# Performance work log

Hardware: AMD Instinct MI355X
Metric: run time of the kernel (lower is better)

## Reference

```python
import jax, jax.numpy as jnp
import numpy as np

EP = 1e-4
EPMAX = 30.0
RTOL, ATOL = 1e-5, 1e-8  # torch.allclose defaults


def _safe(n):
    return jnp.where(n == 0, 1.0, n)


def _rigid_from_3(x):
    # x: (L, 3, 3) -> rot (L,3,3) rows e1,e2,e3 ; origin (L,3)
    x1, x2, x3 = x[:, 0], x[:, 1], x[:, 2]
    v1 = x3 - x2
    v2 = x1 - x2
    e1 = v1 / (jnp.linalg.norm(v1, axis=-1, keepdims=True) + 1e-3)
    u2 = v2 - e1 * jnp.einsum('ld,ld->l', e1, v2)[:, None]
    e2 = u2 / (jnp.linalg.norm(u2, axis=-1, keepdims=True) + 1e-8)
    e3 = jnp.cross(e1, e2)
    return jnp.stack([e1, e2, e3], axis=1), x2


def _merge_frames(rot, trans, ii, jj):
    # Vectorized merge_coordinate_systems over all selected pairs (ii, jj).
    O_A, O_B = trans[ii], trans[jj]          # (P,3)
    RA, RB = rot[ii], rot[jj]                # (P,3,3)
    close = jnp.all(jnp.abs(O_A - O_B) <= ATOL + RTOL * jnp.abs(O_B), axis=-1)
    d = O_B - O_A
    nd = jnp.linalg.norm(d, axis=-1)
    X_new = d / _safe(nd)[:, None]
    Z_add = RA[:, 2] + RB[:, 2]
    Z_sub = RA[:, 2] - RB[:, 2]
    na = jnp.linalg.norm(Z_add, axis=-1)
    ns = jnp.linalg.norm(Z_sub, axis=-1)
    Z_new = jnp.where((na > ns)[:, None], Z_add / _safe(na)[:, None], Z_sub / _safe(ns)[:, None])
    Y_new = jnp.cross(Z_new, X_new)
    nan_bad = jnp.any(jnp.isnan(Y_new), axis=-1)
    flip = jnp.einsum('pd,pd->p', jnp.cross(X_new, Y_new), Z_new) < 0
    Y_new = jnp.where(flip[:, None], -Y_new, Y_new)
    R_new = jnp.stack([X_new, Y_new, Z_new], axis=1)  # (P,3,3)
    O_new = 0.5 * (O_A + O_B)
    bad = close | (nd == 0) | (na == 0) | (ns == 0) | nan_bad
    R_out = jnp.where(bad[:, None, None], RA, R_new)
    O_out = jnp.where(bad[:, None], O_A, O_new)
    return jnp.concatenate([rot, R_out], axis=0), jnp.concatenate([trans, O_out], axis=0)


def _frame_transform(points, rot, tran):
    # points: (N,3); rot: (F,3,3); tran: (F,3) -> (N,F,3)
    diff = points[:, None, :] - tran[None, :, :]
    return jnp.einsum('nfd,fed->nfe', diff, rot)


def setup_inputs():
    key = jax.random.key(0)
    k0, k1, k2, k3 = jax.random.split(key, 4)
    L = 1024
    coor = 5.0 * jax.random.normal(k0, (L, 3, 3), jnp.float32)
    # valid orthonormal frames from random points
    rot, _ = _rigid_from_3(5.0 * jax.random.normal(k1, (L, 3, 3), jnp.float32))
    trans = 5.0 * jax.random.normal(k2, (L, 3), jnp.float32)
    target = 5.0 * jax.random.normal(k3, (L, 3, 3), jnp.float32)
    idx = np.arange(L)
    band = idx[None, :] - idx[:, None]
    matrix = ((band > 0) & (band <= 8)).astype(np.int32)  # ~8k contact pairs
    return {"coor": coor, "rot": rot, "trans": trans, "target": target,
            "matrix": jnp.asarray(matrix)}


def reference(coor, rot, trans, target, matrix):
    m = np.asarray(matrix)
    ii_np, jj_np = np.nonzero(np.triu(m, 1) == 1)
    ii, jj = jnp.asarray(ii_np), jnp.asarray(jj_np)
    p_rot, p_tran = _merge_frames(rot, trans, ii, jj)
    pred_x2 = _frame_transform(coor.reshape(-1, 3), p_rot, p_tran)   # (N,F,3)
    t_rot0, t_tran0 = _rigid_from_3(target)
    t_rot, t_tran = _merge_frames(t_rot0, t_tran0, ii, jj)
    tx = _frame_transform(target.reshape(-1, 3), t_rot, t_tran)     # (N,F,3)
    errmap = jnp.sqrt(jnp.sum((pred_x2 - tx) ** 2 + EP, axis=-1))
    return jnp.mean(jnp.minimum(errmap, EPMAX))
```

## Files before the change

kernel.cpp:

```cpp
#include <hip/hip_runtime.h>

#define EPV    0.0001f
#define EPMAXV 30.0f
#define RTOLV  1e-5f
#define ATOLV  1e-8f
#define NPART  1024
#define CHUNK  112

#define PIN(x) asm volatile("" : "+v"(x))


__device__ inline void write_rec(float* __restrict__ rec,
                                 const float Rp[9], const float Op[3],
                                 const float Rt[9], const float Ot[3]) {
    float P[9], N[9];
#pragma unroll
    for (int k = 0; k < 9; k++) { P[k] = Rp[k]; N[k] = -Rt[k]; }
    float kx = -(P[0] * Op[0] + P[1] * Op[1] + P[2] * Op[2]
               + N[0] * Ot[0] + N[1] * Ot[1] + N[2] * Ot[2]);
    float ky = -(P[3] * Op[0] + P[4] * Op[1] + P[5] * Op[2]
               + N[3] * Ot[0] + N[4] * Ot[1] + N[5] * Ot[2]);
    float kz = -(P[6] * Op[0] + P[7] * Op[1] + P[8] * Op[2]
               + N[6] * Ot[0] + N[7] * Ot[1] + N[8] * Ot[2]);
    float4* r4 = (float4*)rec;
    r4[0] = make_float4(P[0], P[1], P[2], P[3]);
    r4[1] = make_float4(P[4], P[5], P[6], P[7]);
    r4[2] = make_float4(P[8], N[0], N[1], N[2]);
    r4[3] = make_float4(N[3], N[4], N[5], N[6]);
    r4[4] = make_float4(N[7], N[8], kx, ky);
    r4[5] = make_float4(kz, 0.f, 0.f, 0.f);
}

__global__ void k_prep(const int* __restrict__ m, int L, unsigned int* __restrict__ rowcnt,
                       const float* __restrict__ rot, const float* __restrict__ trans,
                       const float* __restrict__ target, int nrb,
                       float* __restrict__ pF, float* __restrict__ tF,
                       float* __restrict__ rec) {
    if ((int)blockIdx.x < nrb) {
        int i = blockIdx.x * 4 + (threadIdx.x >> 6);
        if (i >= L) return;
        int lane = threadIdx.x & 63;
        const int4* row4 = (const int4*)(m + (size_t)i * L);
        unsigned int c = 0;
        for (int b = lane; b * 4 < L; b += 64) {
            int4 v = row4[b];
            int j = b * 4;
            c += (unsigned)((j + 0 > i) & (v.x == 1)) + (unsigned)((j + 1 > i) & (v.y == 1))
               + (unsigned)((j + 2 > i) & (v.z == 1)) + (unsigned)((j + 3 > i) & (v.w == 1));
        }
#pragma unroll
        for (int off = 1; off < 64; off <<= 1) c += __shfl_xor(c, off, 64);
        if (lane == 0) rowcnt[i] = c;
        return;
    }
    int l = ((int)blockIdx.x - nrb) * 256 + threadIdx.x;
    if (l >= L) return;
    float Rp[9], Op[3];
#pragma unroll
    for (int k = 0; k < 9; k++) Rp[k] = rot[l * 9 + k];
#pragma unroll
    for (int k = 0; k < 3; k++) Op[k] = trans[l * 3 + k];
    float* pf = pF + l * 12;
#pragma unroll
    for (int k = 0; k < 9; k++) pf[k] = Rp[k];
#pragma unroll
    for (int k = 0; k < 3; k++) pf[9 + k] = Op[k];
    const float* tg = target + l * 9;
    float x1x = tg[0], x1y = tg[1], x1z = tg[2];
    float x2x = tg[3], x2y = tg[4], x2z = tg[5];
    float x3x = tg[6], x3y = tg[7], x3z = tg[8];
    float v1x = x3x - x2x, v1y = x3y - x2y, v1z = x3z - x2z;
    float v2x = x1x - x2x, v2y = x1y - x2y, v2z = x1z - x2z;
    float n1 = sqrtf(v1x * v1x + v1y * v1y + v1z * v1z) + 0.001f;
    float e1x = v1x / n1, e1y = v1y / n1, e1z = v1z / n1;
    float c = e1x * v2x + e1y * v2y + e1z * v2z;
    float u2x = v2x - c * e1x, u2y = v2y - c * e1y, u2z = v2z - c * e1z;
    float n2 = sqrtf(u2x * u2x + u2y * u2y + u2z * u2z) + 1e-8f;
    float e2x = u2x / n2, e2y = u2y / n2, e2z = u2z / n2;
    float Rt[9], Ot[3];
    Rt[0] = e1x; Rt[1] = e1y; Rt[2] = e1z;
    Rt[3] = e2x; Rt[4] = e2y; Rt[5] = e2z;
    Rt[6] = e1y * e2z - e1z * e2y;
    Rt[7] = e1z * e2x - e1x * e2z;
    Rt[8] = e1x * e2y - e1y * e2x;
    Ot[0] = x2x; Ot[1] = x2y; Ot[2] = x2z;
    float* tf = tF + l * 12;
#pragma unroll
    for (int k = 0; k < 9; k++) tf[k] = Rt[k];
#pragma unroll
    for (int k = 0; k < 3; k++) tf[9 + k] = Ot[k];
    write_rec(rec + (size_t)l * 24, Rp, Op, Rt, Ot);
}

__device__ inline void merge_frames(const float* __restrict__ A, const float* __restrict__ B,
                                    float R[9], float O[3]) {
    const float* RA = A; const float* OA = A + 9;
    const float* RB = B; const float* OB = B + 9;
    bool close = (fabsf(OA[0] - OB[0]) <= ATOLV + RTOLV * fabsf(OB[0])) &&
                 (fabsf(OA[1] - OB[1]) <= ATOLV + RTOLV * fabsf(OB[1])) &&
                 (fabsf(OA[2] - OB[2]) <= ATOLV + RTOLV * fabsf(OB[2]));
    float d0 = OB[0] - OA[0], d1 = OB[1] - OA[1], d2 = OB[2] - OA[2];
    float nd = sqrtf(d0 * d0 + d1 * d1 + d2 * d2);
    float nds = (nd == 0.f) ? 1.f : nd;
    float X0 = d0 / nds, X1 = d1 / nds, X2 = d2 / nds;
    float Za0 = RA[6] + RB[6], Za1 = RA[7] + RB[7], Za2 = RA[8] + RB[8];
    float Zs0 = RA[6] - RB[6], Zs1 = RA[7] - RB[7], Zs2 = RA[8] - RB[8];
    float na = sqrtf(Za0 * Za0 + Za1 * Za1 + Za2 * Za2);
    float ns = sqrtf(Zs0 * Zs0 + Zs1 * Zs1 + Zs2 * Zs2);
    float nas = (na == 0.f) ? 1.f : na;
    float nss = (ns == 0.f) ? 1.f : ns;
    float Z0, Z1, Z2;
    if (na > ns) { Z0 = Za0 / nas; Z1 = Za1 / nas; Z2 = Za2 / nas; }
    else         { Z0 = Zs0 / nss; Z1 = Zs1 / nss; Z2 = Zs2 / nss; }
    float Y0 = Z1 * X2 - Z2 * X1;
    float Y1 = Z2 * X0 - Z0 * X2;
    float Y2 = Z0 * X1 - Z1 * X0;
    bool nanbad = (Y0 != Y0) || (Y1 != Y1) || (Y2 != Y2);
    float C0 = X1 * Y2 - X2 * Y1;
    float C1 = X2 * Y0 - X0 * Y2;
    float C2 = X0 * Y1 - X1 * Y0;
    float dotv = C0 * Z0 + C1 * Z1 + C2 * Z2;
    if (dotv < 0.f) { Y0 = -Y0; Y1 = -Y1; Y2 = -Y2; }
    bool bad = close || (nd == 0.f) || (na == 0.f) || (ns == 0.f) || nanbad;
    if (bad) {
#pragma unroll
        for (int k = 0; k < 9; k++) R[k] = RA[k];
#pragma unroll
        for (int k = 0; k < 3; k++) O[k] = OA[k];
    } else {
        R[0] = X0; R[1] = X1; R[2] = X2;
        R[3] = Y0; R[4] = Y1; R[5] = Y2;
        R[6] = Z0; R[7] = Z1; R[8] = Z2;
        O[0] = 0.5f * (OA[0] + OB[0]);
        O[1] = 0.5f * (OA[1] + OB[1]);
        O[2] = 0.5f * (OA[2] + OB[2]);
    }
}

__global__ void k_fillmerge(const int* __restrict__ m, int L,
                            const unsigned int* __restrict__ rowcnt,
                            unsigned int* __restrict__ count, int cap,
                            const float* __restrict__ pF, const float* __restrict__ tF,
                            float* __restrict__ rec) {
    int i = blockIdx.x * 4 + (threadIdx.x >> 6);
    int lane = threadIdx.x & 63;

    if (blockIdx.x == 0 && (threadIdx.x >> 6) == 0) {
        unsigned int t = 0;
        for (int r = lane; r < L; r += 64) t += rowcnt[r];
#pragma unroll
        for (int off = 1; off < 64; off <<= 1) t += __shfl_xor(t, off, 64);
        if (lane == 0) *count = t;
    }
    if (i >= L) return;

    unsigned int p = 0;
    for (int r = lane; r < i; r += 64) p += rowcnt[r];
#pragma unroll
    for (int off = 1; off < 64; off <<= 1) p += __shfl_xor(p, off, 64);
    unsigned int base = p;

    const int* row = m + (size_t)i * L;
    unsigned long long lt = (lane == 0) ? 0ull : ((1ull << lane) - 1ull);
    for (int j0 = 0; j0 < L; j0 += 64) {
        int j = j0 + lane;
        bool v = (j < L) && (j > i) && (row[j] == 1);
        unsigned long long b = __ballot(v);
        if (v) {
            unsigned int pos = base + (unsigned int)__popcll(b & lt);
            if (pos < (unsigned int)cap) {
                float Rp[9], Op[3], Rt[9], Ot[3];
                merge_frames(pF + i * 12, pF + j * 12, Rp, Op);
                merge_frames(tF + i * 12, tF + j * 12, Rt, Ot);
                write_rec(rec + (size_t)(L + pos) * 24, Rp, Op, Rt, Ot);
            }
        }
        base += (unsigned int)__popcll(b);
    }
}

__global__ __launch_bounds__(256, 4)
void k_main(const float* __restrict__ coor, const float* __restrict__ target,
            const float* __restrict__ rec, const unsigned int* __restrict__ count,
            int cap, int L, int Npts, double* __restrict__ partials) {
    __shared__ float4 sC[CHUNK];
    __shared__ float4 sT[CHUNK];
    __shared__ float sRed[4];
    unsigned int cnt = *count;
    if (cnt > (unsigned int)cap) cnt = (unsigned int)cap;
    int F = L + (int)cnt;
    int nfb = (F + 255) >> 8;
    int nyc = (Npts + CHUNK - 1) / CHUNK;
    int total = nfb * nyc;
    float a0 = 0.f, a1 = 0.f;

    for (int chunk = blockIdx.x; chunk < total; chunk += gridDim.x) {
        int fb = chunk % nfb;
        int yc = chunk / nfb;
        int n0 = yc * CHUNK;
        int npts = Npts - n0; if (npts > CHUNK) npts = CHUNK;
        __syncthreads();
        for (int idx = threadIdx.x; idx < npts; idx += 256) {
            int g = (n0 + idx) * 3;
            sC[idx] = make_float4(coor[g], coor[g + 1], coor[g + 2], 0.f);
            sT[idx] = make_float4(target[g], target[g + 1], target[g + 2], 0.f);
        }
        __syncthreads();
        int f = fb * 256 + threadIdx.x;
        if (f >= F) continue;

        const float4* fr = (const float4*)(rec + (size_t)f * 24);
        float4 r0 = fr[0], r1 = fr[1], r2 = fr[2], r3 = fr[3], r4 = fr[4], r5 = fr[5];
        float P00 = r0.x, P01 = r0.y, P02 = r0.z;
        float P10 = r0.w, P11 = r1.x, P12 = r1.y;
        float P20 = r1.z, P21 = r1.w, P22 = r2.x;
        float N00 = r2.y, N01 = r2.z, N02 = r2.w;
        float N10 = r3.x, N11 = r3.y, N12 = r3.z;
        float N20 = r3.w, N21 = r4.x, N22 = r4.y;
        float kx  = r4.z, ky  = r4.w, kz  = r5.x;
        PIN(P00); PIN(P01); PIN(P02); PIN(P10); PIN(P11); PIN(P12);
        PIN(P20); PIN(P21); PIN(P22);
        PIN(N00); PIN(N01); PIN(N02); PIN(N10); PIN(N11); PIN(N12);
        PIN(N20); PIN(N21); PIN(N22);
        PIN(kx);  PIN(ky);  PIN(kz);

#pragma unroll 4
        for (int n = 0; n < npts; n++) {
            float4 c = sC[n];
            float4 t = sT[n];
            float ux = kx + P00 * c.x + P01 * c.y + P02 * c.z
                          + N00 * t.x + N01 * t.y + N02 * t.z;
            float uy = ky + P10 * c.x + P11 * c.y + P12 * c.z
                          + N10 * t.x + N11 * t.y + N12 * t.z;
            float uz = kz + P20 * c.x + P21 * c.y + P22 * c.z
                          + N20 * t.x + N21 * t.y + N22 * t.z;
            float s = ux * ux + uy * uy + uz * uz + 3.0f * EPV;
            float r = fminf(__builtin_amdgcn_sqrtf(s), EPMAXV);
            if (n & 1) a1 += r; else a0 += r;
        }
    }

    float a = a0 + a1;
#pragma unroll
    for (int off = 32; off > 0; off >>= 1) a += __shfl_down(a, off, 64);
    int lane = threadIdx.x & 63, wv = threadIdx.x >> 6;
    if (lane == 0) sRed[wv] = a;
    __syncthreads();
    if (threadIdx.x == 0)
        partials[blockIdx.x] = (double)(sRed[0] + sRed[1] + sRed[2] + sRed[3]);
}

__global__ void k_final(const double* __restrict__ partials, int npart,
                        const unsigned int* __restrict__ count, int cap,
                        int L, int Npts, float* __restrict__ out) {
    __shared__ double sR[4];
    double d = 0.0;
    for (int i = threadIdx.x; i < npart; i += 256) d += partials[i];
#pragma unroll
    for (int off = 32; off > 0; off >>= 1) d += __shfl_down(d, off, 64);
    int lane = threadIdx.x & 63, wv = threadIdx.x >> 6;
    if (lane == 0) sR[wv] = d;
    __syncthreads();
    if (threadIdx.x == 0) {
        double tot = sR[0] + sR[1] + sR[2] + sR[3];
        unsigned int cnt = *count;
        if (cnt > (unsigned int)cap) cnt = (unsigned int)cap;
        double F = (double)(L + (int)cnt);
        out[0] = (float)(tot / ((double)Npts * F));
    }
}

extern "C" void kernel_launch(void* const* d_in, const int* in_sizes, int n_in,
                              void* d_out, int out_size, void* d_ws, size_t ws_size,
                              hipStream_t stream) {
    const float* coor   = (const float*)d_in[0];
    const float* rot    = (const float*)d_in[1];
    const float* trans  = (const float*)d_in[2];
    const float* target = (const float*)d_in[3];
    const int*   matrix = (const int*)d_in[4];
    int L    = in_sizes[2] / 3;
    int Npts = 3 * L;

    char* ws = (char*)d_ws;
    size_t off = 16;
    unsigned int* count  = (unsigned int*)ws;
    unsigned int* rowcnt = (unsigned int*)(ws + off); off += 4 * (size_t)L;
    off = (off + 15) & ~(size_t)15;
    double* partials = (double*)(ws + off); off += 8 * (size_t)NPART;
    off = (off + 15) & ~(size_t)15;
    float* pF = (float*)(ws + off); off += 48 * (size_t)L;
    float* tF = (float*)(ws + off); off += 48 * (size_t)L;
    off = (off + 15) & ~(size_t)15;
    long cap_ws = ((long)ws_size - (long)off - 96L * (long)L) / 96;
    long capl = cap_ws < 32768 ? cap_ws : 32768;
    if (capl < 0) capl = 0;
    int cap = (int)capl;
    float* rec = (float*)(ws + off);

    int nrb   = (L + 3) / 4;
    int nbase = (L + 255) / 256;
    k_prep<<<nrb + nbase, 256, 0, stream>>>(matrix, L, rowcnt, rot, trans, target,
                                            nrb, pF, tF, rec);
    k_fillmerge<<<nrb, 256, 0, stream>>>(matrix, L, rowcnt, count, cap, pF, tF, rec);
    k_main<<<NPART, 256, 0, stream>>>(coor, target, rec, count, cap, L, Npts, partials);
    k_final<<<1, 256, 0, stream>>>(partials, NPART, count, cap, L, Npts, (float*)d_out);
}
```

Before: 102.4 us.

## Fuse final reduction into main kernel and vectorize fillmerge row scan

Drops the separate k_final launch. The last k_main block to finish, found with an atomic counter plus thread fences, now reduces the per-block partials and writes the output. The counter is reset inside k_prep. The fillmerge row scan now reads the matrix as int4 and computes write slots with a wave prefix scan instead of scalar loads with ballot, which cuts iterations and load instructions. This saves one kernel launch and speeds up compaction, at the cost of an atomic and the serialized tail work in the last block.

```diff
diff --git a/kernel.cpp b/kernel.cpp
--- a/kernel.cpp
+++ b/kernel.cpp
@@ -35,7 +35,8 @@
                        const float* __restrict__ rot, const float* __restrict__ trans,
                        const float* __restrict__ target, int nrb,
                        float* __restrict__ pF, float* __restrict__ tF,
-                       float* __restrict__ rec) {
+                       float* __restrict__ rec, unsigned int* __restrict__ done) {
+    if (blockIdx.x == 0 && threadIdx.x == 0) *done = 0u;
     if ((int)blockIdx.x < nrb) {
         int i = blockIdx.x * 4 + (threadIdx.x >> 6);
         if (i >= L) return;
@@ -160,32 +161,52 @@
     for (int off = 1; off < 64; off <<= 1) p += __shfl_xor(p, off, 64);
     unsigned int base = p;
 
-    const int* row = m + (size_t)i * L;
-    unsigned long long lt = (lane == 0) ? 0ull : ((1ull << lane) - 1ull);
-    for (int j0 = 0; j0 < L; j0 += 64) {
-        int j = j0 + lane;
-        bool v = (j < L) && (j > i) && (row[j] == 1);
-        unsigned long long b = __ballot(v);
-        if (v) {
-            unsigned int pos = base + (unsigned int)__popcll(b & lt);
-            if (pos < (unsigned int)cap) {
-                float Rp[9], Op[3], Rt[9], Ot[3];
-                merge_frames(pF + i * 12, pF + j * 12, Rp, Op);
-                merge_frames(tF + i * 12, tF + j * 12, Rt, Ot);
-                write_rec(rec + (size_t)(L + pos) * 24, Rp, Op, Rt, Ot);
+    const int4* row4 = (const int4*)(m + (size_t)i * L);
+    for (int b = lane; b * 4 < L; b += 64) {
+        int4 v = row4[b];
+        int j = b * 4;
+        unsigned h0 = (unsigned)((j + 0 > i) & (v.x == 1));
+        unsigned h1 = (unsigned)((j + 1 > i) & (v.y == 1));
+        unsigned h2 = (unsigned)((j + 2 > i) & (v.z == 1));
+        unsigned h3 = (unsigned)((j + 3 > i) & (v.w == 1));
+        unsigned hc = h0 + h1 + h2 + h3;
+        unsigned inc = hc;
+#pragma unroll
+        for (int off = 1; off < 64; off <<= 1) {
+            unsigned t = __shfl_up(inc, off, 64);
+            if (lane >= off) inc += t;
+        }
+        unsigned slot = base + (inc - hc);
+        if (hc) {
+#pragma unroll
+            for (int k = 0; k < 4; k++) {
+                unsigned hk = (k == 0) ? h0 : (k == 1) ? h1 : (k == 2) ? h2 : h3;
+                if (hk) {
+                    int jj = j + k;
+                    if (slot < (unsigned int)cap) {
+                        float Rp[9], Op[3], Rt[9], Ot[3];
+                        merge_frames(pF + i * 12, pF + jj * 12, Rp, Op);
+                        merge_frames(tF + i * 12, tF + jj * 12, Rt, Ot);
+                        write_rec(rec + (size_t)(L + slot) * 24, Rp, Op, Rt, Ot);
+                    }
+                    slot++;
+                }
             }
         }
-        base += (unsigned int)__popcll(b);
+        base += __shfl(inc, 63, 64);
     }
 }
 
 __global__ __launch_bounds__(256, 4)
 void k_main(const float* __restrict__ coor, const float* __restrict__ target,
             const float* __restrict__ rec, const unsigned int* __restrict__ count,
-            int cap, int L, int Npts, double* __restrict__ partials) {
+            int cap, int L, int Npts, double* __restrict__ partials,
+            unsigned int* __restrict__ done, float* __restrict__ out) {
     __shared__ float4 sC[CHUNK];
     __shared__ float4 sT[CHUNK];
     __shared__ float sRed[4];
+    __shared__ int sLast;
+    __shared__ double sRd[4];
     unsigned int cnt = *count;
     if (cnt > (unsigned int)cap) cnt = (unsigned int)cap;
     int F = L + (int)cnt;
@@ -246,27 +267,25 @@
     int lane = threadIdx.x & 63, wv = threadIdx.x >> 6;
     if (lane == 0) sRed[wv] = a;
     __syncthreads();
-    if (threadIdx.x == 0)
+    if (threadIdx.x == 0) {
         partials[blockIdx.x] = (double)(sRed[0] + sRed[1] + sRed[2] + sRed[3]);
-}
-
-__global__ void k_final(const double* __restrict__ partials, int npart,
-                        const unsigned int* __restrict__ count, int cap,
-                        int L, int Npts, float* __restrict__ out) {
-    __shared__ double sR[4];
-    double d = 0.0;
-    for (int i = threadIdx.x; i < npart; i += 256) d += partials[i];
-#pragma unroll
-    for (int off = 32; off > 0; off >>= 1) d += __shfl_down(d, off, 64);
-    int lane = threadIdx.x & 63, wv = threadIdx.x >> 6;
-    if (lane == 0) sR[wv] = d;
+        __threadfence();
+        unsigned int prev = atomicAdd(done, 1u);
+        sLast = (prev == gridDim.x - 1u) ? 1 : 0;
+    }
     __syncthreads();
-    if (threadIdx.x == 0) {
-        double tot = sR[0] + sR[1] + sR[2] + sR[3];
-        unsigned int cnt = *count;
-        if (cnt > (unsigned int)cap) cnt = (unsigned int)cap;
-        double F = (double)(L + (int)cnt);
-        out[0] = (float)(tot / ((double)Npts * F));
+    if (sLast) {
+        __threadfence();
+        double d = 0.0;
+        for (int i = threadIdx.x; i < (int)gridDim.x; i += 256) d += partials[i];
+#pragma unroll
+        for (int off = 32; off > 0; off >>= 1) d += __shfl_down(d, off, 64);
+        if (lane == 0) sRd[wv] = d;
+        __syncthreads();
+        if (threadIdx.x == 0) {
+            double tot = sRd[0] + sRd[1] + sRd[2] + sRd[3];
+            out[0] = (float)(tot / ((double)Npts * (double)F));
+        }
     }
 }
 
@@ -284,6 +303,7 @@
     char* ws = (char*)d_ws;
     size_t off = 16;
     unsigned int* count  = (unsigned int*)ws;
+    unsigned int* done   = (unsigned int*)(ws + 4);
     unsigned int* rowcnt = (unsigned int*)(ws + off); off += 4 * (size_t)L;
     off = (off + 15) & ~(size_t)15;
     double* partials = (double*)(ws + off); off += 8 * (size_t)NPART;
@@ -300,8 +320,8 @@
     int nrb   = (L + 3) / 4;
     int nbase = (L + 255) / 256;
     k_prep<<<nrb + nbase, 256, 0, stream>>>(matrix, L, rowcnt, rot, trans, target,
-                                            nrb, pF, tF, rec);
+                                            nrb, pF, tF, rec, done);
     k_fillmerge<<<nrb, 256, 0, stream>>>(matrix, L, rowcnt, count, cap, pF, tF, rec);
-    k_main<<<NPART, 256, 0, stream>>>(coor, target, rec, count, cap, L, Npts, partials);
-    k_final<<<1, 256, 0, stream>>>(partials, NPART, count, cap, L, Npts, (float*)d_out);
-}
+    k_main<<<NPART, 256, 0, stream>>>(coor, target, rec, count, cap, L, Npts,
+                                      partials, done, (float*)d_out);
+}
```

New measurement: 118.3 us. 15.6% more time.
